# Optimization experiments

Measured on AMD Instinct MI355X. Metric: run time of the kernel, lower is better.

Reference implementation:

```python
import jax, jax.numpy as jnp
import numpy as np

N_BIT = 8
Q_SCALE = float(1 << N_BIT)        # 256
Q_MAX = (1 << N_BIT) - 1           # 255
MASK = (1 << N_BIT) - 1            # keep only low n_bit bits (carry out of bit 7 dropped)
STRIDE = 1
PADDING = 1


def _quant(x):
    # torch: (x * 2**n_bit).clamp(0, 255).to(int32) -- truncation toward zero; nonneg after clamp
    return jnp.clip(x * Q_SCALE, 0.0, float(Q_MAX)).astype(jnp.int32)


def _im2col(x, k, stride, padding):
    # F.unfold equivalent; patches: [N, C*k*k, h_out, w_out] with channel-major (C, kh, kw) ordering
    patches = jax.lax.conv_general_dilated_patches(
        x, (k, k), (stride, stride), [(padding, padding), (padding, padding)],
        dimension_numbers=("NCHW", "OIHW", "NCHW"))
    N, K, h_out, w_out = patches.shape
    L = h_out * w_out
    # torch: view(N, K, L).permute(1, 2, 0).reshape(K, L*N)
    X_col = patches.reshape(N, K, L).transpose(1, 2, 0).reshape(K, L * N)
    return X_col, h_out, w_out


def _adder_fwd_math(W_col, X_col):
    # mode='logic', table=None => approx full adder is an EXACT full adder over n_bit=8 bits,
    # i.e. (qa + qb) mod 256, then /256, then -sum(|.|) over the K (im2col) axis.
    a = _quant(W_col)[:, :, None]     # [F, K, 1]
    b = _quant(X_col)[None, :, :]     # [1, K, M]
    s = (a + b) & MASK                # [F, K, M] int32
    return -jnp.sum(jnp.abs(s.astype(jnp.float32) / Q_SCALE), axis=1)  # [F, M]


def setup_inputs() -> dict:
    key = jax.random.key(0)
    k1, k2 = jax.random.split(key)
    x = jax.random.normal(k1, (8, 32, 32, 32), dtype=jnp.float32)   # [N, C, H, W]
    W = jax.random.normal(k2, (32, 32, 3, 3), dtype=jnp.float32)    # [F, C, k, k]
    return {"x": x, "W": W}


def reference(x, W):
    F_, C, kh, kw = W.shape
    N = x.shape[0]
    X_col, h_out, w_out = _im2col(x, kh, STRIDE, PADDING)   # [K, L*N]
    W_col = W.reshape(F_, C * kh * kw)                       # [F, K]
    out = _adder_fwd_math(W_col, X_col)                      # [F, L*N]
    out = out.reshape(F_, h_out, w_out, N).transpose(3, 0, 1, 2)  # [N, F, h_out, w_out]
    return out
```

## Files before the change

### kernel.cpp

```cpp
#include <hip/hip_runtime.h>

#define NHB 0x7f7f7f7fu
#define HIB 0x80808080u

#if __has_builtin(__builtin_amdgcn_sad_u8)
__device__ __forceinline__ unsigned sad8(unsigned a, unsigned b, unsigned c) {
    return __builtin_amdgcn_sad_u8(a, b, c);
}
#else
__device__ __forceinline__ unsigned sad8(unsigned a, unsigned b, unsigned c) {
    unsigned d;
    asm("v_sad_u8 %0, %1, %2, %3" : "=v"(d) : "v"(a), "v"(b), "v"(c));
    return d;
}
#endif

__device__ __forceinline__ unsigned quantq(float v) {
    v = v * 256.0f;
    v = fminf(fmaxf(v, 0.0f), 255.0f);
    return (unsigned)v;
}

__device__ __forceinline__ unsigned pack4(float a, float b, float c, float d) {
    return quantq(a) | (quantq(b) << 8) | (quantq(c) << 16) | (quantq(d) << 24);
}

__global__ __launch_bounds__(1024) void adder2d_kernel(
    const float* __restrict__ x, const float* __restrict__ W,
    float* __restrict__ out)
{
    const int tid = threadIdx.x;
    const int bid = blockIdx.x;
    const int n = bid >> 5;
    const int i = bid & 31;

    __shared__ unsigned sQW[32 * 72];
    __shared__ unsigned sQX[32 * 96];
    __shared__ unsigned sRowW[768];

    {
        const float4* W4 = (const float4*)W;
        for (int m = tid; m < 2304; m += 1024) {
            float4 w = W4[m];
            sQW[m] = pack4(w.x, w.y, w.z, w.w);
        }
    }
    if (tid < 768) {
        int m = tid;
        int c = m / 24;
        int r = m - c * 24;
        int kh = r >> 3;
        int wq = (r & 7) << 2;
        int row = i + kh - 1;
        unsigned pv = 0;
        if (row >= 0 && row < 32) {
            float4 v = *(const float4*)&x[((n * 32 + c) * 32 + row) * 32 + wq];
            pv = pack4(v.x, v.y, v.z, v.w);
        }
        sRowW[m] = pv;
    }
    __syncthreads();

    {
        const unsigned char* sRow = (const unsigned char*)sRowW;
        for (int m = tid; m < 2304; m += 1024) {
            int j = m / 72;
            int p = m - j * 72;
            unsigned v = 0;
#pragma unroll
            for (int e = 0; e < 4; ++e) {
                int k = 4 * p + e;
                int c = k / 9;
                int rem = k - 9 * c;
                int kh = rem / 3;
                int kw = rem - 3 * kh;
                int col = j + kw - 1;
                unsigned bv = (col >= 0 && col < 32) ? (unsigned)sRow[c * 96 + kh * 32 + col] : 0u;
                v |= bv << (8 * e);
            }
            int g = p >> 2, e2 = p & 3;
            sQX[j * 96 + (((g ^ (j & 7)) << 2) + e2)] = v;
        }
    }
    __syncthreads();

    const int f = tid >> 5;
    const int j = tid & 31;
    const int js = j & 7;
    const uint4* qwr = (const uint4*)&sQW[f * 72];
    const uint4* qxr = (const uint4*)&sQX[j * 96];
    unsigned acc = 0;
#pragma unroll 6
    for (int g = 0; g < 18; ++g) {
        uint4 a = qwr[g];
        uint4 b = qxr[g ^ js];
        acc = sad8(((a.x & NHB) + (b.x & NHB)) ^ ((a.x ^ b.x) & HIB), 0u, acc);
        acc = sad8(((a.y & NHB) + (b.y & NHB)) ^ ((a.y ^ b.y) & HIB), 0u, acc);
        acc = sad8(((a.z & NHB) + (b.z & NHB)) ^ ((a.z ^ b.z) & HIB), 0u, acc);
        acc = sad8(((a.w & NHB) + (b.w & NHB)) ^ ((a.w ^ b.w) & HIB), 0u, acc);
    }

    out[((n * 32 + f) * 32 + i) * 32 + j] = -(float)acc * (1.0f / 256.0f);
}

extern "C" void kernel_launch(void* const* d_in, const int* in_sizes, int n_in,
                              void* d_out, int out_size, void* d_ws, size_t ws_size,
                              hipStream_t stream) {
    const float* x = (const float*)d_in[0];
    const float* W = (const float*)d_in[1];
    float* out = (float*)d_out;
    adder2d_kernel<<<256, 1024, 0, stream>>>(x, W, out);
}
```

Measured before the change: 11.97 us.

## Split each output row across two blocks of 512 threads

Each block now handles half of an output row (16 columns) for all 32 filters, which doubles the grid to 512 blocks of 512 threads. The aim is to spread work over more CUs on the 256-CU part and to shrink per-block shared memory for the packed input. The cost is that every block still quantizes all of W and the three input rows, so that redundant setup work doubles. The inner K loop is also fully unrolled.

```diff
diff --git a/kernel.cpp b/kernel.cpp
--- a/kernel.cpp
+++ b/kernel.cpp
@@ -25,32 +25,33 @@
     return quantq(a) | (quantq(b) << 8) | (quantq(c) << 16) | (quantq(d) << 24);
 }
 
-__global__ __launch_bounds__(1024) void adder2d_kernel(
+__global__ __launch_bounds__(512) void adder2d_kernel(
     const float* __restrict__ x, const float* __restrict__ W,
     float* __restrict__ out)
 {
     const int tid = threadIdx.x;
     const int bid = blockIdx.x;
-    const int n = bid >> 5;
-    const int i = bid & 31;
+    const int n  = bid >> 6;
+    const int r  = bid & 63;
+    const int i  = r >> 1;
+    const int jh = (r & 1) << 4;
 
-    __shared__ unsigned sQW[32 * 72];
-    __shared__ unsigned sQX[32 * 96];
+    __shared__ unsigned sQW[2304];
+    __shared__ unsigned sQX[16 * 96];
     __shared__ unsigned sRowW[768];
 
     {
         const float4* W4 = (const float4*)W;
-        for (int m = tid; m < 2304; m += 1024) {
+        for (int m = tid; m < 2304; m += 512) {
             float4 w = W4[m];
             sQW[m] = pack4(w.x, w.y, w.z, w.w);
         }
     }
-    if (tid < 768) {
-        int m = tid;
+    for (int m = tid; m < 768; m += 512) {
         int c = m / 24;
-        int r = m - c * 24;
-        int kh = r >> 3;
-        int wq = (r & 7) << 2;
+        int rr = m - c * 24;
+        int kh = rr >> 3;
+        int wq = (rr & 7) << 2;
         int row = i + kh - 1;
         unsigned pv = 0;
         if (row >= 0 && row < 32) {
@@ -63,9 +64,10 @@
 
     {
         const unsigned char* sRow = (const unsigned char*)sRowW;
-        for (int m = tid; m < 2304; m += 1024) {
-            int j = m / 72;
-            int p = m - j * 72;
+        for (int m = tid; m < 1152; m += 512) {
+            int jj = m / 72;
+            int p = m - jj * 72;
+            int j = jh + jj;
             unsigned v = 0;
 #pragma unroll
             for (int e = 0; e < 4; ++e) {
@@ -79,18 +81,18 @@
                 v |= bv << (8 * e);
             }
             int g = p >> 2, e2 = p & 3;
-            sQX[j * 96 + (((g ^ (j & 7)) << 2) + e2)] = v;
+            sQX[jj * 96 + (((g ^ (jj & 7)) << 2) + e2)] = v;
         }
     }
     __syncthreads();
 
-    const int f = tid >> 5;
-    const int j = tid & 31;
-    const int js = j & 7;
+    const int f = tid >> 4;
+    const int jl = tid & 15;
+    const int js = jl & 7;
     const uint4* qwr = (const uint4*)&sQW[f * 72];
-    const uint4* qxr = (const uint4*)&sQX[j * 96];
+    const uint4* qxr = (const uint4*)&sQX[jl * 96];
     unsigned acc = 0;
-#pragma unroll 6
+#pragma unroll
     for (int g = 0; g < 18; ++g) {
         uint4 a = qwr[g];
         uint4 b = qxr[g ^ js];
@@ -100,7 +102,7 @@
         acc = sad8(((a.w & NHB) + (b.w & NHB)) ^ ((a.w ^ b.w) & HIB), 0u, acc);
     }
 
-    out[((n * 32 + f) * 32 + i) * 32 + j] = -(float)acc * (1.0f / 256.0f);
+    out[((n * 32 + f) * 32 + i) * 32 + jh + jl] = -(float)acc * (1.0f / 256.0f);
 }
 
 extern "C" void kernel_launch(void* const* d_in, const int* in_sizes, int n_in,
@@ -109,5 +111,5 @@
     const float* x = (const float*)d_in[0];
     const float* W = (const float*)d_in[1];
     float* out = (float*)d_out;
-    adder2d_kernel<<<256, 1024, 0, stream>>>(x, W, out);
+    adder2d_kernel<<<512, 512, 0, stream>>>(x, W, out);
 }
```

Result: no change. 12.03 us (+0.5%).
